# Optimization experiments

Hardware: AMD Instinct MI355X
Metric: run time of the kernel (lower is better)

Reference implementation:

```python
import jax, jax.numpy as jnp
import numpy as np

D_MODEL = 1024
NUM_HEADS = 16
HEAD_DIM = D_MODEL // NUM_HEADS
B, N = 4, 2048


def setup_inputs() -> dict:
    key = jax.random.key(0)
    ks = jax.random.split(key, 9)
    s = 1.0 / np.sqrt(D_MODEL)
    inp = {
        "x": jax.random.normal(ks[0], (B, N, D_MODEL), dtype=jnp.float32),
        "Wq": jax.random.normal(ks[1], (D_MODEL, D_MODEL), dtype=jnp.float32) * s,
        "bq": jnp.zeros((D_MODEL,), dtype=jnp.float32),
        "Wk": jax.random.normal(ks[2], (D_MODEL, D_MODEL), dtype=jnp.float32) * s,
        "bk": jnp.zeros((D_MODEL,), dtype=jnp.float32),
        "Wv": jax.random.normal(ks[3], (D_MODEL, D_MODEL), dtype=jnp.float32) * s,
        "bv": jnp.zeros((D_MODEL,), dtype=jnp.float32),
        "Wo": jax.random.normal(ks[4], (D_MODEL, D_MODEL), dtype=jnp.float32) * s,
        "bo": jnp.zeros((D_MODEL,), dtype=jnp.float32),
    }
    return inp


def reference(x, Wq, bq, Wk, bk, Wv, bv, Wo, bo):
    b, n, c = x.shape
    h, d = NUM_HEADS, HEAD_DIM
    # QKV projections -> [B, H, N, d]
    q = (x @ Wq + bq).reshape(b, n, h, d).transpose(0, 2, 1, 3)
    k = (x @ Wk + bk).reshape(b, n, h, d).transpose(0, 2, 1, 3)
    v = (x @ Wv + bv).reshape(b, n, h, d).transpose(0, 2, 1, 3)
    scores = jnp.einsum("bhqd,bhkd->bhqk", q, k) / np.sqrt(d).astype(jnp.float32)
    attn = jax.nn.softmax(scores, axis=-1)  # dropout p=0 -> identity
    out = jnp.einsum("bhqk,bhkd->bhqd", attn, v)
    out = out.transpose(0, 2, 1, 3).reshape(b, n, c)
    return out @ Wo + bo
```

## Files before the change

### kernel.cpp

```cpp
#include <hip/hip_runtime.h>
#include <hip/hip_bf16.h>
#include <stdint.h>

#define DM 1024
#define SEQL 2048
#define NBATCH 4
#define NHEAD 16
#define HDIM 64
#define MTOT (NBATCH * SEQL)

using f32x4 = __attribute__((ext_vector_type(4))) float;
using f32x16 = __attribute__((ext_vector_type(16))) float;
using bf16x8 = __attribute__((ext_vector_type(8))) short;

static __device__ __forceinline__ unsigned short f2bf(float f) {
  union { float f; uint32_t u; } v; v.f = f;
  uint32_t u = v.u;
  return (unsigned short)((u + 0x7FFFu + ((u >> 16) & 1u)) >> 16);
}

static __device__ __forceinline__ float exp2_fast(float x) {
#if __has_builtin(__builtin_amdgcn_exp2f)
  return __builtin_amdgcn_exp2f(x);
#else
  float r;
  asm("v_exp_f32 %0, %1" : "=v"(r) : "v"(x));
  return r;
#endif
}

static __device__ __forceinline__ uint32_t pkbf(float lo, float hi) {
  float2 f; f.x = lo; f.y = hi;
  __hip_bfloat162 h = __float22bfloat162_rn(f);
  union { __hip_bfloat162 h; uint32_t u; } cv; cv.h = h;
  return cv.u;
}

static __device__ __forceinline__ f32x16 zero16() {
  f32x16 z;
#pragma unroll
  for (int i = 0; i < 16; ++i) z[i] = 0.f;
  return z;
}

static __device__ __forceinline__ void gload16(const void* g, void* l) {
  __builtin_amdgcn_global_load_lds(
      (const __attribute__((address_space(1))) unsigned int*)g,
      (__attribute__((address_space(3))) unsigned int*)l,
      16, 0, 0);
}

__global__ __launch_bounds__(256) void transpose_convert4(
    const float* __restrict__ W0, const float* __restrict__ W1,
    const float* __restrict__ W2, const float* __restrict__ W3,
    unsigned short* __restrict__ T0, unsigned short* __restrict__ T1,
    unsigned short* __restrict__ T2, unsigned short* __restrict__ T3) {
  __shared__ float tile[64][65];
  const int z = blockIdx.z;
  const float* W = z == 0 ? W0 : z == 1 ? W1 : z == 2 ? W2 : W3;
  unsigned short* WT = z == 0 ? T0 : z == 1 ? T1 : z == 2 ? T2 : T3;
  const int bx = blockIdx.x;
  const int by = blockIdx.y;
  const int t = threadIdx.x;
  const int r = t >> 4;
  const int c4 = (t & 15) * 4;
#pragma unroll
  for (int i = 0; i < 4; ++i) {
    const float4 v = *reinterpret_cast<const float4*>(
        &W[(size_t)(by * 64 + r + i * 16) * DM + bx * 64 + c4]);
    tile[r + i * 16][c4 + 0] = v.x;
    tile[r + i * 16][c4 + 1] = v.y;
    tile[r + i * 16][c4 + 2] = v.z;
    tile[r + i * 16][c4 + 3] = v.w;
  }
  __syncthreads();
#pragma unroll
  for (int i = 0; i < 4; ++i) {
    const int rr = r + i * 16;
    uint32_t lo = (uint32_t)f2bf(tile[c4 + 0][rr]) | ((uint32_t)f2bf(tile[c4 + 1][rr]) << 16);
    uint32_t hi = (uint32_t)f2bf(tile[c4 + 2][rr]) | ((uint32_t)f2bf(tile[c4 + 3][rr]) << 16);
    uint2 o; o.x = lo; o.y = hi;
    *reinterpret_cast<uint2*>(&WT[(size_t)(bx * 64 + rr) * DM + by * 64 + c4]) = o;
  }
}

__global__ __launch_bounds__(256) void convert_x(
    const float* __restrict__ x, unsigned short* __restrict__ xb) {
  const int i = blockIdx.x * 256 + threadIdx.x;
  const float4 v = reinterpret_cast<const float4*>(x)[i];
  uint2 o;
  o.x = (uint32_t)f2bf(v.x) | ((uint32_t)f2bf(v.y) << 16);
  o.y = (uint32_t)f2bf(v.z) | ((uint32_t)f2bf(v.w) << 16);
  reinterpret_cast<uint2*>(xb)[i] = o;
}

#define QSCALE 0.1803368801111204f

__global__ __launch_bounds__(256) void gemm_qkv(
    const unsigned short* __restrict__ A, const unsigned short* __restrict__ BT,
    const float* __restrict__ bq, const float* __restrict__ bk, const float* __restrict__ bv,
    unsigned short* __restrict__ qo, unsigned short* __restrict__ ko,
    unsigned short* __restrict__ vo) {
  __shared__ unsigned short As[128][64];
  __shared__ unsigned short Bs[128][64];
  const int tid = threadIdx.x;
  const int w = tid >> 6;
  const int lane = tid & 63;
  const int wm = w >> 1, wn = w & 1;
  const int m0 = blockIdx.y * 128;
  const int n0 = blockIdx.x * 128;
  const int mode = n0 >> 10;
  const int lrow = lane & 15;
  const int lk = (lane >> 4) * 8;
  const int sRow = lane >> 3;
  const int sCol = (lane & 7) * 8;

  unsigned short* dstA = (mode == 2) ? &Bs[0][0] : &As[0][0];
  unsigned short* dstB = (mode == 2) ? &As[0][0] : &Bs[0][0];

  f32x4 acc[4][4];
#pragma unroll
  for (int m = 0; m < 4; ++m)
#pragma unroll
    for (int n = 0; n < 4; ++n) acc[m][n] = (f32x4){0.f, 0.f, 0.f, 0.f};

  for (int k0 = 0; k0 < DM; k0 += 64) {
#pragma unroll
    for (int i = 0; i < 4; ++i) {
      const int rb = i * 32 + w * 8;
      gload16(&A[(size_t)(m0 + rb + sRow) * DM + k0 + sCol], dstA + rb * 64);
    }
#pragma unroll
    for (int i = 0; i < 4; ++i) {
      const int rb = i * 32 + w * 8;
      gload16(&BT[(size_t)(n0 + rb + sRow) * DM + k0 + sCol], dstB + rb * 64);
    }
    __syncthreads();
#pragma unroll
    for (int ks = 0; ks < 2; ++ks) {
      bf16x8 af[4], bfr[4];
#pragma unroll
      for (int m = 0; m < 4; ++m)
        af[m] = *reinterpret_cast<const bf16x8*>(&As[wm * 64 + m * 16 + lrow][ks * 32 + lk]);
#pragma unroll
      for (int n = 0; n < 4; ++n)
        bfr[n] = *reinterpret_cast<const bf16x8*>(&Bs[wn * 64 + n * 16 + lrow][ks * 32 + lk]);
#pragma unroll
      for (int m = 0; m < 4; ++m)
#pragma unroll
        for (int n = 0; n < 4; ++n)
          acc[m][n] = __builtin_amdgcn_mfma_f32_16x16x32_bf16(af[m], bfr[n], acc[m][n], 0, 0, 0);
    }
    __syncthreads();
  }

  if (mode < 2) {
    const bool isK = (mode == 1);
    unsigned short* dst = isK ? ko : qo;
    const float* bp = isK ? bk : bq;
    const float sc = isK ? 1.f : QSCALE;
#pragma unroll
    for (int n = 0; n < 4; ++n) {
      const int col = (n0 & 1023) + wn * 64 + n * 16 + lrow;
      const float bb = bp[col];
      const int hh = col >> 6, dd = col & 63;
#pragma unroll
      for (int m = 0; m < 4; ++m) {
        const int rowb = m0 + wm * 64 + m * 16 + (lane >> 4) * 4;
#pragma unroll
        for (int r = 0; r < 4; ++r) {
          const int mg = rowb + r;
          const int bidx = mg >> 11;
          const int nn = mg & 2047;
          dst[((size_t)(bidx * NHEAD + hh) * SEQL + nn) * HDIM + dd] =
              f2bf((acc[m][n][r] + bb) * sc);
        }
      }
    }
  } else {
#pragma unroll
    for (int m = 0; m < 4; ++m) {
#pragma unroll
      for (int r = 0; r < 4; ++r) {
        const int dv = (n0 - 2048) + wm * 64 + m * 16 + (lane >> 4) * 4 + r;
        const float bb = bv[dv];
        const int hh = dv >> 6, dd = dv & 63;
#pragma unroll
        for (int n = 0; n < 4; ++n) {
          const int seq = m0 + wn * 64 + n * 16 + lrow;
          const int bidx = seq >> 11;
          const int nn = seq & 2047;
          vo[((size_t)(bidx * NHEAD + hh) * HDIM + dd) * SEQL + nn] =
              f2bf(acc[m][n][r] + bb);
        }
      }
    }
  }
}

__global__ __launch_bounds__(256) void gemm_out(
    const unsigned short* __restrict__ A, const unsigned short* __restrict__ BT,
    const float* __restrict__ bias, float* __restrict__ Cout) {
  __shared__ unsigned short As[128][64];
  __shared__ unsigned short Bs[128][64];
  const int tid = threadIdx.x;
  const int w = tid >> 6;
  const int lane = tid & 63;
  const int wm = w >> 1, wn = w & 1;
  const int m0 = (blockIdx.x >> 3) * 128;
  const int n0 = (blockIdx.x & 7) * 128;
  const int lrow = lane & 15;
  const int lk = (lane >> 4) * 8;
  const int sRow = lane >> 3;
  const int sCol = (lane & 7) * 8;

  f32x4 acc[4][4];
#pragma unroll
  for (int m = 0; m < 4; ++m)
#pragma unroll
    for (int n = 0; n < 4; ++n) acc[m][n] = (f32x4){0.f, 0.f, 0.f, 0.f};

  for (int k0 = 0; k0 < DM; k0 += 64) {
#pragma unroll
    for (int i = 0; i < 4; ++i) {
      const int rb = i * 32 + w * 8;
      gload16(&A[(size_t)(m0 + rb + sRow) * DM + k0 + sCol], &As[rb][0]);
    }
#pragma unroll
    for (int i = 0; i < 4; ++i) {
      const int rb = i * 32 + w * 8;
      gload16(&BT[(size_t)(n0 + rb + sRow) * DM + k0 + sCol], &Bs[rb][0]);
    }
    __syncthreads();
#pragma unroll
    for (int ks = 0; ks < 2; ++ks) {
      bf16x8 af[4], bfr[4];
#pragma unroll
      for (int m = 0; m < 4; ++m)
        af[m] = *reinterpret_cast<const bf16x8*>(&As[wm * 64 + m * 16 + lrow][ks * 32 + lk]);
#pragma unroll
      for (int n = 0; n < 4; ++n)
        bfr[n] = *reinterpret_cast<const bf16x8*>(&Bs[wn * 64 + n * 16 + lrow][ks * 32 + lk]);
#pragma unroll
      for (int m = 0; m < 4; ++m)
#pragma unroll
        for (int n = 0; n < 4; ++n)
          acc[m][n] = __builtin_amdgcn_mfma_f32_16x16x32_bf16(af[m], bfr[n], acc[m][n], 0, 0, 0);
    }
    __syncthreads();
  }

#pragma unroll
  for (int n = 0; n < 4; ++n) {
    const int col = n0 + wn * 64 + n * 16 + lrow;
    const float bb = bias[col];
#pragma unroll
    for (int m = 0; m < 4; ++m) {
      const int rowb = m0 + wm * 64 + m * 16 + (lane >> 4) * 4;
#pragma unroll
      for (int r = 0; r < 4; ++r) {
        Cout[(size_t)(rowb + r) * DM + col] = acc[m][n][r] + bb;
      }
    }
  }
}

__global__ __launch_bounds__(512) void attn_kernel(
    const unsigned short* __restrict__ q, const unsigned short* __restrict__ k,
    const unsigned short* __restrict__ vt, unsigned short* __restrict__ attn_out) {
  __shared__ unsigned short Ks[2][64 * 64];
  __shared__ unsigned short Vs[2][64 * 64];

  const int bid = blockIdx.x;
  const int l0 = (bid & 7) * 64 + (bid >> 3);
  const int bh = l0 >> 3;
  const int qt = l0 & 7;
  const int b = bh >> 4, h = bh & 15;

  const int tid = threadIdx.x;
  const int w = tid >> 6;
  const int lane = tid & 63;
  const int qv = lane & 31;
  const int hi = lane >> 5;
  const int qg0 = qt * 256 + w * 32;

  const unsigned short* qptr = q + (size_t)bh * SEQL * HDIM;
  const unsigned short* kptr = k + (size_t)bh * SEQL * HDIM;
  const unsigned short* vptr = vt + (size_t)bh * HDIM * SEQL;

  bf16x8 qb[4];
#pragma unroll
  for (int kc = 0; kc < 4; ++kc)
    qb[kc] = *reinterpret_cast<const bf16x8*>(&qptr[(qg0 + qv) * HDIM + kc * 16 + hi * 8]);

  bf16x8 ones;
#pragma unroll
  for (int i = 0; i < 8; ++i) ones[i] = (short)0x3F80;

  f32x16 acc0 = zero16(), acc1 = zero16(), accL = zero16();

  const int x7 = qv & 7;
  int off[4];
#pragma unroll
  for (int i = 0; i < 4; ++i) off[i] = ((2 * i + hi) ^ x7) << 3;

  const int srow = tid >> 3;
  const int sslot = tid & 7;
  const int sdst = srow * 64 + ((sslot ^ (srow & 7)) << 3);

  uint4 rk, rv;
#define LOADT(t)                                                                    \
  {                                                                                 \
    rk = *reinterpret_cast<const uint4*>(&kptr[((t) * 64 + srow) * HDIM + sslot * 8]); \
    rv = *reinterpret_cast<const uint4*>(&vptr[srow * SEQL + (t) * 64 + sslot * 8]);   \
  }

  LOADT(0);
  const int NT = SEQL / 64;
  for (int t = 0; t < NT; ++t) {
    const int c = t & 1;
    *reinterpret_cast<uint4*>(&Ks[c][sdst]) = rk;
    *reinterpret_cast<uint4*>(&Vs[c][sdst]) = rv;
    __syncthreads();
    if (t + 1 < NT) LOADT(t + 1);

    f32x16 p0 = zero16(), p1 = zero16();
    __builtin_amdgcn_s_setprio(1);
#pragma unroll
    for (int kc = 0; kc < 4; ++kc) {
      bf16x8 ka0 = *reinterpret_cast<const bf16x8*>(&Ks[c][qv * 64 + off[kc]]);
      bf16x8 ka1 = *reinterpret_cast<const bf16x8*>(&Ks[c][(32 + qv) * 64 + off[kc]]);
      p0 = __builtin_amdgcn_mfma_f32_32x32x16_bf16(ka0, qb[kc], p0, 0, 0, 0);
      p1 = __builtin_amdgcn_mfma_f32_32x32x16_bf16(ka1, qb[kc], p1, 0, 0, 0);
    }
    __builtin_amdgcn_s_setprio(0);

#pragma unroll
    for (int i = 0; i < 16; ++i) {
      p0[i] = exp2_fast(p0[i]);
      p1[i] = exp2_fast(p1[i]);
    }

    bf16x8 pa[4];
#pragma unroll
    for (int ks = 0; ks < 4; ++ks) {
      const int o = 8 * (ks & 1);
      uint32_t X1, X2, Y1, Y2;
      if (ks < 2) {
        X1 = pkbf(p0[o + 0], p0[o + 1]); X2 = pkbf(p0[o + 2], p0[o + 3]);
        Y1 = pkbf(p0[o + 4], p0[o + 5]); Y2 = pkbf(p0[o + 6], p0[o + 7]);
      } else {
        X1 = pkbf(p1[o + 0], p1[o + 1]); X2 = pkbf(p1[o + 2], p1[o + 3]);
        Y1 = pkbf(p1[o + 4], p1[o + 5]); Y2 = pkbf(p1[o + 6], p1[o + 7]);
      }
      asm("v_permlane32_swap_b32 %0, %1" : "+v"(X1), "+v"(Y1));
      asm("v_permlane32_swap_b32 %0, %1" : "+v"(X2), "+v"(Y2));
      union { uint32_t u[4]; bf16x8 v; } uu;
      uu.u[0] = X1; uu.u[1] = X2; uu.u[2] = Y1; uu.u[3] = Y2;
      pa[ks] = uu.v;
    }

    __builtin_amdgcn_s_setprio(1);
#pragma unroll
    for (int ks = 0; ks < 4; ++ks) {
      bf16x8 vb0 = *reinterpret_cast<const bf16x8*>(&Vs[c][qv * 64 + off[ks]]);
      bf16x8 vb1 = *reinterpret_cast<const bf16x8*>(&Vs[c][(32 + qv) * 64 + off[ks]]);
      acc0 = __builtin_amdgcn_mfma_f32_32x32x16_bf16(pa[ks], vb0, acc0, 0, 0, 0);
      acc1 = __builtin_amdgcn_mfma_f32_32x32x16_bf16(pa[ks], vb1, acc1, 0, 0, 0);
      accL = __builtin_amdgcn_mfma_f32_32x32x16_bf16(pa[ks], ones, accL, 0, 0, 0);
    }
    __builtin_amdgcn_s_setprio(0);
  }
#undef LOADT

#pragma unroll
  for (int rg = 0; rg < 16; ++rg) {
    const int crow = (rg & 3) + 8 * (rg >> 2) + 4 * hi;
    const float invl = 1.f / accL[rg];
    const int qg = qg0 + crow;
    const size_t base = ((size_t)(b * SEQL + qg) * NHEAD + h) * HDIM + qv;
    attn_out[base] = f2bf(acc0[rg] * invl);
    attn_out[base + 32] = f2bf(acc1[rg] * invl);
  }
}

extern "C" void kernel_launch(void* const* d_in, const int* in_sizes, int n_in,
                              void* d_out, int out_size, void* d_ws, size_t ws_size,
                              hipStream_t stream) {
  const float* x  = (const float*)d_in[0];
  const float* Wq = (const float*)d_in[1];
  const float* bq = (const float*)d_in[2];
  const float* Wk = (const float*)d_in[3];
  const float* bk = (const float*)d_in[4];
  const float* Wv = (const float*)d_in[5];
  const float* bv = (const float*)d_in[6];
  const float* Wo = (const float*)d_in[7];
  const float* bo = (const float*)d_in[8];

  char* ws = (char*)d_ws;
  unsigned short* wqT = (unsigned short*)(ws);
  unsigned short* wkT = wqT + 1024 * 1024;
  unsigned short* wvT = wkT + 1024 * 1024;
  unsigned short* woT = wvT + 1024 * 1024;
  unsigned short* xb   = (unsigned short*)(ws + (size_t)(8 << 20));
  unsigned short* attn = xb;
  unsigned short* qw   = (unsigned short*)(ws + (size_t)(24 << 20));
  unsigned short* kw   = (unsigned short*)(ws + (size_t)(40 << 20));
  unsigned short* vtw  = (unsigned short*)(ws + (size_t)(56 << 20));

  transpose_convert4<<<dim3(16, 16, 4), 256, 0, stream>>>(Wq, Wk, Wv, Wo, wqT, wkT, wvT, woT);
  convert_x<<<MTOT * DM / 4 / 256, 256, 0, stream>>>(x, xb);

  gemm_qkv<<<dim3(24, 64), 256, 0, stream>>>(xb, wqT, bq, bk, bv, qw, kw, vtw);

  attn_kernel<<<512, 512, 0, stream>>>(qw, kw, vtw, attn);

  gemm_out<<<512, 256, 0, stream>>>(attn, woT, bo, (float*)d_out);
}
```

Measured before the change: 204.6 us.

## Replace QKV and output GEMMs with pipelined 256x128 swizzled-LDS GEMM template

Replaces the two 128x128 GEMM kernels with a templated 512-thread kernel that computes 256x128 tiles using a 4-deep LDS ring buffer. Global-to-LDS loads run two stages ahead, with manual vmcnt waits and a single barrier per K step. LDS layout is XOR-swizzled to avoid bank conflicts, and MFMA sections get raised priority. The QKV GEMM is split into a Q/K launch and a separate V launch with swapped operands, and blocks are remapped for XCD locality. The cost is more LDS and register use per block, which may lower occupancy.

```diff
diff --git a/kernel.cpp b/kernel.cpp
--- a/kernel.cpp
+++ b/kernel.cpp
@@ -96,27 +96,52 @@
 
 #define QSCALE 0.1803368801111204f
 
-__global__ __launch_bounds__(256) void gemm_qkv(
-    const unsigned short* __restrict__ A, const unsigned short* __restrict__ BT,
-    const float* __restrict__ bq, const float* __restrict__ bk, const float* __restrict__ bv,
-    unsigned short* __restrict__ qo, unsigned short* __restrict__ ko,
-    unsigned short* __restrict__ vo) {
-  __shared__ unsigned short As[128][64];
-  __shared__ unsigned short Bs[128][64];
+template <int MODE, int NNT>
+__global__ __launch_bounds__(512) void gemm_big(
+    const unsigned short* __restrict__ A, const unsigned short* __restrict__ B,
+    const float* __restrict__ bias0, const float* __restrict__ bias1,
+    void* __restrict__ out0, void* __restrict__ out1) {
+  __shared__ unsigned short Abuf[4][256 * 32];
+  __shared__ unsigned short Bbuf[4][128 * 32];
+
   const int tid = threadIdx.x;
   const int w = tid >> 6;
   const int lane = tid & 63;
-  const int wm = w >> 1, wn = w & 1;
-  const int m0 = blockIdx.y * 128;
-  const int n0 = blockIdx.x * 128;
-  const int mode = n0 >> 10;
+
+  const int cpx = gridDim.x >> 3;
+  const int bid = (blockIdx.x & 7) * cpx + (blockIdx.x >> 3);
+  const int m0 = (bid / NNT) * 256;
+  const int n0 = (bid % NNT) * 128;
+
+  const int srow = tid >> 2;
+  const int scol = (((lane & 3) ^ ((lane >> 3) & 3))) << 3;
+  unsigned short* ldsA0 = &Abuf[0][w * 512];
+  unsigned short* ldsA1 = &Abuf[0][4096 + w * 512];
+  unsigned short* ldsB  = &Bbuf[0][w * 512];
+
+#define STAGE(tt, bb)                                                          \
+  {                                                                            \
+    const int kk = (tt) * 32;                                                  \
+    gload16(&A[(size_t)(m0 + srow) * DM + kk + scol], ldsA0 + (bb) * 8192);    \
+    gload16(&A[(size_t)(m0 + 128 + srow) * DM + kk + scol], ldsA1 + (bb) * 8192); \
+    gload16(&B[(size_t)(n0 + srow) * DM + kk + scol], ldsB + (bb) * 4096);     \
+  }
+
+  const int wm = w >> 1;
+  const int wn = w & 1;
   const int lrow = lane & 15;
-  const int lk = (lane >> 4) * 8;
-  const int sRow = lane >> 3;
-  const int sCol = (lane & 7) * 8;
-
-  unsigned short* dstA = (mode == 2) ? &Bs[0][0] : &As[0][0];
-  unsigned short* dstB = (mode == 2) ? &As[0][0] : &Bs[0][0];
+  const int ls = lane >> 4;
+  int aoff[4], boff[4];
+#pragma unroll
+  for (int m = 0; m < 4; ++m) {
+    const int r = wm * 64 + m * 16 + lrow;
+    aoff[m] = r * 32 + ((ls ^ ((r >> 1) & 3)) << 3);
+  }
+#pragma unroll
+  for (int n = 0; n < 4; ++n) {
+    const int r = wn * 64 + n * 16 + lrow;
+    boff[n] = r * 32 + ((ls ^ ((r >> 1) & 3)) << 3);
+  }
 
   f32x4 acc[4][4];
 #pragma unroll
@@ -124,40 +149,46 @@
 #pragma unroll
     for (int n = 0; n < 4; ++n) acc[m][n] = (f32x4){0.f, 0.f, 0.f, 0.f};
 
-  for (int k0 = 0; k0 < DM; k0 += 64) {
-#pragma unroll
-    for (int i = 0; i < 4; ++i) {
-      const int rb = i * 32 + w * 8;
-      gload16(&A[(size_t)(m0 + rb + sRow) * DM + k0 + sCol], dstA + rb * 64);
-    }
-#pragma unroll
-    for (int i = 0; i < 4; ++i) {
-      const int rb = i * 32 + w * 8;
-      gload16(&BT[(size_t)(n0 + rb + sRow) * DM + k0 + sCol], dstB + rb * 64);
-    }
-    __syncthreads();
-#pragma unroll
-    for (int ks = 0; ks < 2; ++ks) {
-      bf16x8 af[4], bfr[4];
-#pragma unroll
-      for (int m = 0; m < 4; ++m)
-        af[m] = *reinterpret_cast<const bf16x8*>(&As[wm * 64 + m * 16 + lrow][ks * 32 + lk]);
+  STAGE(0, 0);
+  STAGE(1, 1);
+  asm volatile("s_waitcnt vmcnt(3)" ::: "memory");
+  __builtin_amdgcn_s_barrier();
+
+  const int NK = DM / 32;
+  for (int t = 0; t < NK; ++t) {
+    const int b = t & 3;
+    if (t + 2 < NK) STAGE(t + 2, (t + 2) & 3);
+
+    bf16x8 af[4], bfr[4];
+#pragma unroll
+    for (int m = 0; m < 4; ++m)
+      af[m] = *reinterpret_cast<const bf16x8*>(&Abuf[b][aoff[m]]);
+#pragma unroll
+    for (int n = 0; n < 4; ++n)
+      bfr[n] = *reinterpret_cast<const bf16x8*>(&Bbuf[b][boff[n]]);
+
+    __builtin_amdgcn_s_setprio(1);
+#pragma unroll
+    for (int m = 0; m < 4; ++m)
 #pragma unroll
       for (int n = 0; n < 4; ++n)
-        bfr[n] = *reinterpret_cast<const bf16x8*>(&Bs[wn * 64 + n * 16 + lrow][ks * 32 + lk]);
-#pragma unroll
-      for (int m = 0; m < 4; ++m)
-#pragma unroll
-        for (int n = 0; n < 4; ++n)
-          acc[m][n] = __builtin_amdgcn_mfma_f32_16x16x32_bf16(af[m], bfr[n], acc[m][n], 0, 0, 0);
-    }
-    __syncthreads();
-  }
-
-  if (mode < 2) {
-    const bool isK = (mode == 1);
-    unsigned short* dst = isK ? ko : qo;
-    const float* bp = isK ? bk : bq;
+        acc[m][n] = __builtin_amdgcn_mfma_f32_16x16x32_bf16(af[m], bfr[n], acc[m][n], 0, 0, 0);
+    __builtin_amdgcn_s_setprio(0);
+
+    asm volatile("s_waitcnt lgkmcnt(0)" ::: "memory");
+    if (t < NK - 2) {
+      asm volatile("s_waitcnt vmcnt(3)" ::: "memory");
+    } else {
+      asm volatile("s_waitcnt vmcnt(0)" ::: "memory");
+    }
+    __builtin_amdgcn_s_barrier();
+  }
+#undef STAGE
+
+  if (MODE == 0) {
+    const int isK = n0 >> 10;
+    unsigned short* dst = isK ? (unsigned short*)out1 : (unsigned short*)out0;
+    const float* bp = isK ? bias1 : bias0;
     const float sc = isK ? 1.f : QSCALE;
 #pragma unroll
     for (int n = 0; n < 4; ++n) {
@@ -166,7 +197,7 @@
       const int hh = col >> 6, dd = col & 63;
 #pragma unroll
       for (int m = 0; m < 4; ++m) {
-        const int rowb = m0 + wm * 64 + m * 16 + (lane >> 4) * 4;
+        const int rowb = m0 + wm * 64 + m * 16 + ls * 4;
 #pragma unroll
         for (int r = 0; r < 4; ++r) {
           const int mg = rowb + r;
@@ -177,89 +208,36 @@
         }
       }
     }
-  } else {
+  } else if (MODE == 1) {
 #pragma unroll
     for (int m = 0; m < 4; ++m) {
 #pragma unroll
       for (int r = 0; r < 4; ++r) {
-        const int dv = (n0 - 2048) + wm * 64 + m * 16 + (lane >> 4) * 4 + r;
-        const float bb = bv[dv];
-        const int hh = dv >> 6, dd = dv & 63;
+        const int ch = m0 + wm * 64 + m * 16 + ls * 4 + r;
+        const float bb = bias0[ch];
+        const int hh = ch >> 6, dd = ch & 63;
 #pragma unroll
         for (int n = 0; n < 4; ++n) {
-          const int seq = m0 + wn * 64 + n * 16 + lrow;
-          const int bidx = seq >> 11;
-          const int nn = seq & 2047;
-          vo[((size_t)(bidx * NHEAD + hh) * HDIM + dd) * SEQL + nn] =
+          const int sq = n0 + wn * 64 + n * 16 + lrow;
+          const int bidx = sq >> 11;
+          const int nn = sq & 2047;
+          ((unsigned short*)out0)[((size_t)(bidx * NHEAD + hh) * HDIM + dd) * SEQL + nn] =
               f2bf(acc[m][n][r] + bb);
         }
       }
     }
-  }
-}
-
-__global__ __launch_bounds__(256) void gemm_out(
-    const unsigned short* __restrict__ A, const unsigned short* __restrict__ BT,
-    const float* __restrict__ bias, float* __restrict__ Cout) {
-  __shared__ unsigned short As[128][64];
-  __shared__ unsigned short Bs[128][64];
-  const int tid = threadIdx.x;
-  const int w = tid >> 6;
-  const int lane = tid & 63;
-  const int wm = w >> 1, wn = w & 1;
-  const int m0 = (blockIdx.x >> 3) * 128;
-  const int n0 = (blockIdx.x & 7) * 128;
-  const int lrow = lane & 15;
-  const int lk = (lane >> 4) * 8;
-  const int sRow = lane >> 3;
-  const int sCol = (lane & 7) * 8;
-
-  f32x4 acc[4][4];
-#pragma unroll
-  for (int m = 0; m < 4; ++m)
-#pragma unroll
-    for (int n = 0; n < 4; ++n) acc[m][n] = (f32x4){0.f, 0.f, 0.f, 0.f};
-
-  for (int k0 = 0; k0 < DM; k0 += 64) {
-#pragma unroll
-    for (int i = 0; i < 4; ++i) {
-      const int rb = i * 32 + w * 8;
-      gload16(&A[(size_t)(m0 + rb + sRow) * DM + k0 + sCol], &As[rb][0]);
-    }
-#pragma unroll
-    for (int i = 0; i < 4; ++i) {
-      const int rb = i * 32 + w * 8;
-      gload16(&BT[(size_t)(n0 + rb + sRow) * DM + k0 + sCol], &Bs[rb][0]);
-    }
-    __syncthreads();
-#pragma unroll
-    for (int ks = 0; ks < 2; ++ks) {
-      bf16x8 af[4], bfr[4];
-#pragma unroll
-      for (int m = 0; m < 4; ++m)
-        af[m] = *reinterpret_cast<const bf16x8*>(&As[wm * 64 + m * 16 + lrow][ks * 32 + lk]);
-#pragma unroll
-      for (int n = 0; n < 4; ++n)
-        bfr[n] = *reinterpret_cast<const bf16x8*>(&Bs[wn * 64 + n * 16 + lrow][ks * 32 + lk]);
-#pragma unroll
-      for (int m = 0; m < 4; ++m)
-#pragma unroll
-        for (int n = 0; n < 4; ++n)
-          acc[m][n] = __builtin_amdgcn_mfma_f32_16x16x32_bf16(af[m], bfr[n], acc[m][n], 0, 0, 0);
-    }
-    __syncthreads();
-  }
-
-#pragma unroll
-  for (int n = 0; n < 4; ++n) {
-    const int col = n0 + wn * 64 + n * 16 + lrow;
-    const float bb = bias[col];
-#pragma unroll
-    for (int m = 0; m < 4; ++m) {
-      const int rowb = m0 + wm * 64 + m * 16 + (lane >> 4) * 4;
-#pragma unroll
-      for (int r = 0; r < 4; ++r) {
-        Cout[(size_t)(rowb + r) * DM + col] = acc[m][n][r] + bb;
+  } else {
+#pragma unroll
+    for (int n = 0; n < 4; ++n) {
+      const int col = n0 + wn * 64 + n * 16 + lrow;
+      const float bb = bias0[col];
+#pragma unroll
+      for (int m = 0; m < 4; ++m) {
+        const int rowb = m0 + wm * 64 + m * 16 + ls * 4;
+#pragma unroll
+        for (int r = 0; r < 4; ++r) {
+          ((float*)out0)[(size_t)(rowb + r) * DM + col] = acc[m][n][r] + bb;
+        }
       }
     }
   }
@@ -411,9 +389,10 @@
   transpose_convert4<<<dim3(16, 16, 4), 256, 0, stream>>>(Wq, Wk, Wv, Wo, wqT, wkT, wvT, woT);
   convert_x<<<MTOT * DM / 4 / 256, 256, 0, stream>>>(x, xb);
 
-  gemm_qkv<<<dim3(24, 64), 256, 0, stream>>>(xb, wqT, bq, bk, bv, qw, kw, vtw);
+  gemm_big<0, 16><<<512, 512, 0, stream>>>(xb, wqT, bq, bk, qw, kw);
+  gemm_big<1, 64><<<256, 512, 0, stream>>>(wvT, xb, bv, nullptr, vtw, nullptr);
 
   attn_kernel<<<512, 512, 0, stream>>>(qw, kw, vtw, attn);
 
-  gemm_out<<<512, 256, 0, stream>>>(attn, woT, bo, (float*)d_out);
-}
+  gemm_big<2, 8><<<256, 512, 0, stream>>>(attn, woT, bo, nullptr, (float*)d_out, nullptr);
+}
```

Result: slower. 225.2 us (+10.0%).

## Rewrite QKV GEMM with 256x256 tiles, double-buffered LDS, and swizzled layout

Applied to the files above, without the earlier changes.

Replaces the 128x128 single-buffered QKV projection GEMM with a 512-thread, 256x256-tile kernel. Its K loop double-buffers LDS and issues the next tile's global-to-LDS loads while the current tile's MFMAs run. It also XOR-swizzles LDS columns to avoid bank conflicts, remaps block IDs to group blocks by XCD, and raises MFMA wave priority. The intent is to raise arithmetic intensity and hide load latency, at the cost of much higher LDS (128KB) and register use, which limits occupancy to one block per CU.

```diff
diff --git a/kernel.cpp b/kernel.cpp
--- a/kernel.cpp
+++ b/kernel.cpp
@@ -96,67 +96,104 @@
 
 #define QSCALE 0.1803368801111204f
 
-__global__ __launch_bounds__(256) void gemm_qkv(
-    const unsigned short* __restrict__ A, const unsigned short* __restrict__ BT,
+__global__ __launch_bounds__(512) void gemm_qkv2(
+    const unsigned short* __restrict__ A, const unsigned short* __restrict__ B,
     const float* __restrict__ bq, const float* __restrict__ bk, const float* __restrict__ bv,
-    unsigned short* __restrict__ qo, unsigned short* __restrict__ ko,
-    unsigned short* __restrict__ vo) {
-  __shared__ unsigned short As[128][64];
-  __shared__ unsigned short Bs[128][64];
+    unsigned short* __restrict__ out_q, unsigned short* __restrict__ out_k,
+    unsigned short* __restrict__ out_v) {
+  constexpr int NNT = 12;
+  __shared__ unsigned short Abuf[2][256 * 64];
+  __shared__ unsigned short Bbuf[2][256 * 64];
+
   const int tid = threadIdx.x;
   const int w = tid >> 6;
   const int lane = tid & 63;
-  const int wm = w >> 1, wn = w & 1;
-  const int m0 = blockIdx.y * 128;
-  const int n0 = blockIdx.x * 128;
-  const int mode = n0 >> 10;
   const int lrow = lane & 15;
-  const int lk = (lane >> 4) * 8;
-  const int sRow = lane >> 3;
-  const int sCol = (lane & 7) * 8;
-
-  unsigned short* dstA = (mode == 2) ? &Bs[0][0] : &As[0][0];
-  unsigned short* dstB = (mode == 2) ? &As[0][0] : &Bs[0][0];
-
-  f32x4 acc[4][4];
-#pragma unroll
-  for (int m = 0; m < 4; ++m)
+  const int lhi = lane >> 4;
+  const int wm = w >> 2;
+  const int wn = w & 3;
+
+  const int cpx = gridDim.x >> 3;
+  const int bid = (blockIdx.x & 7) * cpx + (blockIdx.x >> 3);
+  const int m0 = (bid / NNT) * 256;
+  const int n0 = (bid % NNT) * 256;
+
+  const int srow = w * 8 + (lane >> 3);
+  const int sck = (lane & 7) ^ ((lane >> 3) & 7);
+
+#define STAGE_RR(tt, bb, rr)                                                    \
+  {                                                                             \
+    const int kk = (tt) * 64;                                                   \
+    gload16(&A[(size_t)(m0 + (rr) * 64 + srow) * DM + kk + sck * 8],            \
+            (char*)&Abuf[bb][0] + ((rr) * 64 + w * 8) * 128);                   \
+    gload16(&B[(size_t)(n0 + (rr) * 64 + srow) * DM + kk + sck * 8],            \
+            (char*)&Bbuf[bb][0] + ((rr) * 64 + w * 8) * 128);                   \
+  }
+
+  const bool vswap = (n0 >= 2048);
+
+  f32x4 acc[8][4];
+#pragma unroll
+  for (int m = 0; m < 8; ++m)
 #pragma unroll
     for (int n = 0; n < 4; ++n) acc[m][n] = (f32x4){0.f, 0.f, 0.f, 0.f};
 
-  for (int k0 = 0; k0 < DM; k0 += 64) {
-#pragma unroll
-    for (int i = 0; i < 4; ++i) {
-      const int rb = i * 32 + w * 8;
-      gload16(&A[(size_t)(m0 + rb + sRow) * DM + k0 + sCol], dstA + rb * 64);
-    }
-#pragma unroll
-    for (int i = 0; i < 4; ++i) {
-      const int rb = i * 32 + w * 8;
-      gload16(&BT[(size_t)(n0 + rb + sRow) * DM + k0 + sCol], dstB + rb * 64);
-    }
-    __syncthreads();
-#pragma unroll
-    for (int ks = 0; ks < 2; ++ks) {
-      bf16x8 af[4], bfr[4];
-#pragma unroll
-      for (int m = 0; m < 4; ++m)
-        af[m] = *reinterpret_cast<const bf16x8*>(&As[wm * 64 + m * 16 + lrow][ks * 32 + lk]);
-#pragma unroll
-      for (int n = 0; n < 4; ++n)
-        bfr[n] = *reinterpret_cast<const bf16x8*>(&Bs[wn * 64 + n * 16 + lrow][ks * 32 + lk]);
-#pragma unroll
-      for (int m = 0; m < 4; ++m)
-#pragma unroll
-        for (int n = 0; n < 4; ++n)
-          acc[m][n] = __builtin_amdgcn_mfma_f32_16x16x32_bf16(af[m], bfr[n], acc[m][n], 0, 0, 0);
-    }
-    __syncthreads();
-  }
-
-  if (mode < 2) {
-    const bool isK = (mode == 1);
-    unsigned short* dst = isK ? ko : qo;
+  STAGE_RR(0, 0, 0); STAGE_RR(0, 0, 1); STAGE_RR(0, 0, 2); STAGE_RR(0, 0, 3);
+  __syncthreads();
+
+  const int NK = DM / 64;
+  for (int t = 0; t < NK; ++t) {
+    const int bu = t & 1;
+    bf16x8 bfr[4];
+#pragma unroll
+    for (int ph = 0; ph < 4; ++ph) {
+      const int ks = ph >> 1, mh = ph & 1;
+      if (mh == 0) {
+#pragma unroll
+        for (int n = 0; n < 4; ++n) {
+          const int r = wn * 64 + n * 16 + lrow;
+          bfr[n] = *reinterpret_cast<const bf16x8*>(
+              &Bbuf[bu][r * 64 + (((ks * 4 + lhi) ^ (lane & 7)) << 3)]);
+        }
+      }
+      bf16x8 af[4];
+#pragma unroll
+      for (int i = 0; i < 4; ++i) {
+        const int r = wm * 128 + (mh * 4 + i) * 16 + lrow;
+        af[i] = *reinterpret_cast<const bf16x8*>(
+            &Abuf[bu][r * 64 + (((ks * 4 + lhi) ^ (lane & 7)) << 3)]);
+      }
+      if (ph < 2 && t + 1 < NK) {
+        STAGE_RR(t + 1, bu ^ 1, 2 * ph);
+        STAGE_RR(t + 1, bu ^ 1, 2 * ph + 1);
+      }
+      __builtin_amdgcn_s_barrier();
+      __builtin_amdgcn_s_setprio(1);
+      if (vswap) {
+#pragma unroll
+        for (int i = 0; i < 4; ++i)
+#pragma unroll
+          for (int n = 0; n < 4; ++n)
+            acc[mh * 4 + i][n] =
+                __builtin_amdgcn_mfma_f32_16x16x32_bf16(bfr[n], af[i], acc[mh * 4 + i][n], 0, 0, 0);
+      } else {
+#pragma unroll
+        for (int i = 0; i < 4; ++i)
+#pragma unroll
+          for (int n = 0; n < 4; ++n)
+            acc[mh * 4 + i][n] =
+                __builtin_amdgcn_mfma_f32_16x16x32_bf16(af[i], bfr[n], acc[mh * 4 + i][n], 0, 0, 0);
+      }
+      __builtin_amdgcn_s_setprio(0);
+      if (ph == 3) __syncthreads();
+      else __builtin_amdgcn_s_barrier();
+    }
+  }
+#undef STAGE_RR
+
+  if (!vswap) {
+    const int isK = n0 >> 10;
+    unsigned short* dst = isK ? out_k : out_q;
     const float* bp = isK ? bk : bq;
     const float sc = isK ? 1.f : QSCALE;
 #pragma unroll
@@ -165,8 +202,8 @@
       const float bb = bp[col];
       const int hh = col >> 6, dd = col & 63;
 #pragma unroll
-      for (int m = 0; m < 4; ++m) {
-        const int rowb = m0 + wm * 64 + m * 16 + (lane >> 4) * 4;
+      for (int m = 0; m < 8; ++m) {
+        const int rowb = m0 + wm * 128 + m * 16 + lhi * 4;
 #pragma unroll
         for (int r = 0; r < 4; ++r) {
           const int mg = rowb + r;
@@ -178,16 +215,17 @@
       }
     }
   } else {
-#pragma unroll
-    for (int m = 0; m < 4; ++m) {
+    unsigned short* vo = out_v;
+#pragma unroll
+    for (int n = 0; n < 4; ++n) {
 #pragma unroll
       for (int r = 0; r < 4; ++r) {
-        const int dv = (n0 - 2048) + wm * 64 + m * 16 + (lane >> 4) * 4 + r;
-        const float bb = bv[dv];
-        const int hh = dv >> 6, dd = dv & 63;
-#pragma unroll
-        for (int n = 0; n < 4; ++n) {
-          const int seq = m0 + wn * 64 + n * 16 + lrow;
+        const int ch = (n0 - 2048) + wn * 64 + n * 16 + lhi * 4 + r;
+        const float bb = bv[ch];
+        const int hh = ch >> 6, dd = ch & 63;
+#pragma unroll
+        for (int m = 0; m < 8; ++m) {
+          const int seq = m0 + wm * 128 + m * 16 + lrow;
           const int bidx = seq >> 11;
           const int nn = seq & 2047;
           vo[((size_t)(bidx * NHEAD + hh) * HDIM + dd) * SEQL + nn] =
@@ -411,7 +449,7 @@
   transpose_convert4<<<dim3(16, 16, 4), 256, 0, stream>>>(Wq, Wk, Wv, Wo, wqT, wkT, wvT, woT);
   convert_x<<<MTOT * DM / 4 / 256, 256, 0, stream>>>(x, xb);
 
-  gemm_qkv<<<dim3(24, 64), 256, 0, stream>>>(xb, wqT, bq, bk, bv, qw, kw, vtw);
+  gemm_qkv2<<<384, 512, 0, stream>>>(xb, wqT, bq, bk, bv, qw, kw, vtw);
 
   attn_kernel<<<512, 512, 0, stream>>>(qw, kw, vtw, attn);
 
```

After: 339.4 us. 65.8% more time.
